# Optimization experiments

Hardware: AMD Instinct MI355X
Metric: run time of the kernel (lower is better)

Reference implementation:

```python
import jax, jax.numpy as jnp
import numpy as np


def _time_encoding(t, hidden_dim):
    # Sinusoidal continuous-time encoding: t [B,T] -> [B,T,H]
    half = hidden_dim // 2
    freqs = jnp.exp(-jnp.arange(half, dtype=t.dtype) * (np.log(10000.0) / half))
    ang = t[..., None] * freqs  # [B,T,half]
    return jnp.concatenate([jnp.sin(ang), jnp.cos(ang)], axis=-1)


def _gru(x_tbh, w_ih, w_hh, b_ih, b_hh):
    # PyTorch-convention GRU over time-major input [T,B,H]
    B = x_tbh.shape[1]
    H = w_hh.shape[1]
    h0 = jnp.zeros((B, H), x_tbh.dtype)

    def step(h, x):
        gi = x @ w_ih.T + b_ih
        gh = h @ w_hh.T + b_hh
        i_r, i_z, i_n = jnp.split(gi, 3, axis=-1)
        h_r, h_z, h_n = jnp.split(gh, 3, axis=-1)
        r = jax.nn.sigmoid(i_r + h_r)
        z = jax.nn.sigmoid(i_z + h_z)
        n = jnp.tanh(i_n + r * h_n)
        h_new = (1.0 - z) * n + z * h
        return h_new, h_new

    _, ys = jax.lax.scan(step, h0, x_tbh)
    return ys  # [T,B,H]


def setup_inputs():
    key = jax.random.key(0)
    ks = jax.random.split(key, 8)
    B, T, D, H = 32, 256, 64, 128
    x = jax.random.normal(ks[0], (B, T, D), jnp.float32)
    missing_mask = (jax.random.uniform(ks[1], (B, T, D)) < 0.5).astype(jnp.float32)
    visit_time = jnp.cumsum(jax.random.uniform(ks[2], (B, T), jnp.float32) * 2.0, axis=1)
    time_delta = jnp.zeros((B, T), jnp.float32)
    lengths = jax.random.randint(ks[3], (B,), T // 2, T + 1).astype(jnp.int32)
    lengths = lengths.at[0].set(T)  # pad_packed returns max(lengths) steps; pin to T
    sensor_embed = jax.random.normal(ks[4], (D, H), jnp.float32) * 0.02
    k = 1.0 / np.sqrt(H)
    gru_w_ih = jax.random.uniform(ks[5], (3 * H, H), jnp.float32, -k, k)
    gru_w_hh = jax.random.uniform(ks[6], (3 * H, H), jnp.float32, -k, k)
    gru_b_ih = jax.random.uniform(ks[7], (3 * H,), jnp.float32, -k, k)
    gru_b_hh = jnp.zeros((3 * H,), jnp.float32)
    return dict(x=x, missing_mask=missing_mask, visit_time=visit_time,
                time_delta=time_delta, lengths=lengths, sensor_embed=sensor_embed,
                gru_w_ih=gru_w_ih, gru_w_hh=gru_w_hh, gru_b_ih=gru_b_ih, gru_b_hh=gru_b_hh)


def reference(x, missing_mask, visit_time, time_delta, lengths, sensor_embed,
              gru_w_ih, gru_w_hh, gru_b_ih, gru_b_hh):
    B, T, D = x.shape
    H = sensor_embed.shape[1]
    observed = 1.0 - missing_mask                                   # [B,T,D]
    # sensor tokens: per-(t,sensor) embedding scaled by value, zeroed if missing
    sensor_tokens = x[..., None] * sensor_embed[None, None] * observed[..., None]  # [B,T,D,H]
    presence = observed.mean(axis=1)                                # [B,D]
    sim = jax.nn.relu(sensor_embed @ sensor_embed.T)                # [D,D]
    adj = presence[:, :, None] * presence[:, None, :] * sim[None]   # [B,D,D]
    adj = adj + jnp.eye(D, dtype=x.dtype)[None]
    adj = adj / jnp.maximum(adj.sum(axis=-1, keepdims=True), 1e-6)
    graph_tokens = jnp.einsum('bij,btjh->btih', adj, sensor_tokens) # [B,T,D,H]
    visit_repr = graph_tokens.mean(axis=2) + _time_encoding(visit_time, H)  # [B,T,H]
    # dropout is identity in eval mode
    ys = _gru(jnp.swapaxes(visit_repr, 0, 1), gru_w_ih, gru_w_hh, gru_b_ih, gru_b_hh)
    out = jnp.swapaxes(ys, 0, 1)                                    # [B,T,H]
    # pad_packed_sequence semantics: zeros beyond each sequence length
    mask = (jnp.arange(T)[None, :] < lengths[:, None])[..., None]
    return out * mask
```

## Files before the change

kernel.cpp:

```cpp
#include <hip/hip_runtime.h>
#include <hip/hip_bf16.h>

#define B_ 32
#define T_ 256
#define D_ 64
#define H_ 128
#define G_ 384

typedef _Float16 half8 __attribute__((ext_vector_type(8)));
typedef _Float16 half4v __attribute__((ext_vector_type(4)));
typedef float float4v __attribute__((ext_vector_type(4)));

__device__ __forceinline__ float fsigmoid2(float s){
  return __builtin_amdgcn_rcpf(1.0f + __builtin_amdgcn_exp2f(-s));
}
__device__ __forceinline__ float ftanh2(float t){
  return 1.0f - 2.0f*__builtin_amdgcn_rcpf(1.0f + __builtin_amdgcn_exp2f(t));
}
#define LOG2E  1.442695041f
#define LOG2E2 2.885390082f

#define BAR() do{ asm volatile("s_waitcnt lgkmcnt(0)" ::: "memory"); \
                  __builtin_amdgcn_s_barrier(); \
                  asm volatile("" ::: "memory"); } while(0)

__global__ void __launch_bounds__(256) adj_k(const float* mm, const float* E,
                                             float* wcol){
  int b = blockIdx.x;
  int tid = threadIdx.x;
  int d = tid & 63, q = tid >> 6;
  __shared__ float spp[4][64];
  __shared__ float sp[64];
  __shared__ float sE[64*129];
  __shared__ float ssim[64*65];
  __shared__ float srs[64];
  float p = 0.0f;
  for (int t = q*64; t < q*64+64; t++) p += 1.0f - mm[(b*T_ + t)*D_ + d];
  spp[q][d] = p;
  for (int i = tid; i < D_*H_; i += 256){ int r = i >> 7, c = i & 127; sE[r*129+c] = E[i]; }
  __syncthreads();
  if (tid < 64) sp[tid] = (spp[0][tid]+spp[1][tid]+spp[2][tid]+spp[3][tid]) * (1.0f/T_);
  __syncthreads();
  float rowE[128];
  #pragma unroll
  for (int k = 0; k < 128; k++) rowE[k] = sE[d*129+k];
  for (int i = q*16; i < q*16+16; i++){
    float s = 0.0f;
    #pragma unroll
    for (int k = 0; k < 128; k++) s += rowE[k]*sE[i*129+k];
    ssim[d*65+i] = fmaxf(s, 0.0f);
  }
  __syncthreads();
  if (tid < 64){
    float rs = 0.0f;
    for (int j = 0; j < 64; j++) rs += sp[j]*ssim[tid*65+j];
    srs[tid] = fmaxf(sp[tid]*rs + 1.0f, 1e-6f);
  }
  __syncthreads();
  if (tid < 64){
    float s = 0.0f;
    for (int i = 0; i < 64; i++) s += sp[i]*ssim[tid*65+i]/srs[i];
    wcol[b*64 + tid] = sp[tid]*s + 1.0f/srs[tid];
  }
}

#define AVP 72
#define VRP 136
#define SEP 132
__global__ void __launch_bounds__(512,1) gi_k(const float* x, const float* mm,
                                              const float* vt, const float* E,
                                              const float* wih, const float* bih,
                                              const float* bhh, const float* wcol,
                                              _Float16* gi3){
  int bid = blockIdx.x;
  int b = bid >> 3, t0 = (bid & 7)*32;
  int tid = threadIdx.x;
  int w = tid >> 6, l = tid & 63;
  int lq = l >> 4, lm = l & 15;

  __shared__ __align__(16) _Float16 av[32*AVP];
  __shared__ __align__(16) _Float16 vrA[32*VRP];
  __shared__ __align__(16) _Float16 sEl[64*SEP];
  __shared__ float sVt[32];

  {
    int i = tid*4, t = i >> 6, d4 = i & 63;
    long src = (long)(b*T_ + t0 + t)*D_ + d4;
    float4 xv = *(const float4*)&x[src];
    float4 mv = *(const float4*)&mm[src];
    float4 wv = *(const float4*)&wcol[b*D_ + d4];
    half4v h;
    h[0]=(_Float16)(xv.x*(1.0f-mv.x)*wv.x*(1.0f/64));
    h[1]=(_Float16)(xv.y*(1.0f-mv.y)*wv.y*(1.0f/64));
    h[2]=(_Float16)(xv.z*(1.0f-mv.z)*wv.z*(1.0f/64));
    h[3]=(_Float16)(xv.w*(1.0f-mv.w)*wv.w*(1.0f/64));
    *(half4v*)&av[t*AVP + d4] = h;
  }
  {
    int r = tid >> 3, c0 = (tid & 7)*16;
    #pragma unroll
    for (int g = 0; g < 4; g++){
      float4 v = *(const float4*)&E[r*H_ + c0 + g*4];
      half4v h;
      h[0]=(_Float16)v.x; h[1]=(_Float16)v.y; h[2]=(_Float16)v.z; h[3]=(_Float16)v.w;
      *(half4v*)&sEl[r*SEP + c0 + g*4] = h;
    }
  }
  if (tid < 32) sVt[tid] = vt[b*T_ + t0 + tid];
  __syncthreads();

  half8 bE[2];
  #pragma unroll
  for (int kc = 0; kc < 2; kc++){
    half8 f;
    #pragma unroll
    for (int jj = 0; jj < 8; jj++)
      f[jj] = sEl[(kc*32 + lq*8 + jj)*SEP + 16*w + lm];
    bE[kc] = f;
  }

  float4v accA[2] = {{0,0,0,0},{0,0,0,0}};
  #pragma unroll
  for (int kc = 0; kc < 2; kc++){
    #pragma unroll
    for (int mt = 0; mt < 2; mt++){
      half8 a = *(const half8*)&av[(mt*16+lm)*AVP + kc*32 + lq*8];
      accA[mt] = __builtin_amdgcn_mfma_f32_16x16x32_f16(a, bE[kc], accA[mt], 0,0,0);
    }
  }
  {
    int h = 16*w + lm;
    float fr = __expf(-(float)(h & 63) * 0.14391157f);
    #pragma unroll
    for (int mt = 0; mt < 2; mt++){
      #pragma unroll
      for (int r = 0; r < 4; r++){
        int tl = mt*16 + lq*4 + r;
        float ang = sVt[tl] * fr;
        float e = (h < 64) ? __sinf(ang) : __cosf(ang);
        vrA[tl*VRP + h] = (_Float16)(accA[mt][r] + e);
      }
    }
  }
  __syncthreads();

  half8 bW[3][4]; float biW[3];
  #pragma unroll
  for (int q = 0; q < 3; q++){
    int g = 16*(3*w + q) + lm;
    float sc = (g < 2*H_) ? LOG2E : LOG2E2;
    biW[q] = (bih[g] + (g < 2*H_ ? bhh[g] : 0.0f)) * sc;
    #pragma unroll
    for (int kc = 0; kc < 4; kc++){
      const float* src = &wih[(long)g*H_ + kc*32 + lq*8];
      float4 x0 = *(const float4*)src;
      float4 x1 = *(const float4*)(src+4);
      half8 f;
      f[0]=(_Float16)(x0.x*sc); f[1]=(_Float16)(x0.y*sc); f[2]=(_Float16)(x0.z*sc); f[3]=(_Float16)(x0.w*sc);
      f[4]=(_Float16)(x1.x*sc); f[5]=(_Float16)(x1.y*sc); f[6]=(_Float16)(x1.z*sc); f[7]=(_Float16)(x1.w*sc);
      bW[q][kc] = f;
    }
  }
  float4v cB[2][3];
  #pragma unroll
  for (int mt = 0; mt < 2; mt++)
    #pragma unroll
    for (int q = 0; q < 3; q++) cB[mt][q] = (float4v){0,0,0,0};
  #pragma unroll
  for (int kc = 0; kc < 4; kc++){
    #pragma unroll
    for (int mt = 0; mt < 2; mt++){
      half8 a = *(const half8*)&vrA[(mt*16+lm)*VRP + kc*32 + lq*8];
      #pragma unroll
      for (int q = 0; q < 3; q++)
        cB[mt][q] = __builtin_amdgcn_mfma_f32_16x16x32_f16(a, bW[q][kc], cB[mt][q], 0,0,0);
    }
  }
  #pragma unroll
  for (int mt = 0; mt < 2; mt++){
    #pragma unroll
    for (int q = 0; q < 3; q++){
      int g = 16*(3*w + q) + lm;
      int tb = t0 + mt*16 + lq*4;
      half4v hv;
      hv[0]=(_Float16)(cB[mt][q][0] + biW[q]); hv[1]=(_Float16)(cB[mt][q][1] + biW[q]);
      hv[2]=(_Float16)(cB[mt][q][2] + biW[q]); hv[3]=(_Float16)(cB[mt][q][3] + biW[q]);
      *(half4v*)&gi3[((long)(b*G_ + g))*T_ + tb] = hv;
    }
  }
}

__global__ void __launch_bounds__(256,1) gru_k(const _Float16* gi3, const float* whh,
                                               const float* bhh, const int* lengths,
                                               float* out){
  int b = blockIdx.x;
  int tid = threadIdx.x;
  int w = tid >> 6, l = tid & 63;
  int lq = l >> 4, lm = l & 15;
  int len = lengths[b];
  bool gate = (l < 32);
  int j = 32*w + l;

  __shared__ __align__(16) _Float16 hb[2][H_];

  half8 bfrag[6][4];
  #pragma unroll
  for (int i = 0; i < 6; i++){
    int row = 32*w + (i>>1)*H_ + (i&1)*16 + lm;
    float sc = ((i>>1) == 2) ? LOG2E2 : LOG2E;
    #pragma unroll
    for (int kc = 0; kc < 4; kc++){
      const float* src = &whh[(long)row*H_ + kc*32 + lq*8];
      float4 x0 = *(const float4*)src;
      float4 x1 = *(const float4*)(src+4);
      half8 f;
      f[0]=(_Float16)(x0.x*sc); f[1]=(_Float16)(x0.y*sc); f[2]=(_Float16)(x0.z*sc); f[3]=(_Float16)(x0.w*sc);
      f[4]=(_Float16)(x1.x*sc); f[5]=(_Float16)(x1.y*sc); f[6]=(_Float16)(x1.z*sc); f[7]=(_Float16)(x1.w*sc);
      bfrag[i][kc] = f;
    }
  }
  float bn_ = 0.0f;
  const _Float16* pr = nullptr; const _Float16* pz; const _Float16* pn;
  if (gate){
    bn_ = bhh[2*H_ + j] * LOG2E2;
    pr = gi3 + ((long)b*G_ + j)*T_;
    pz = pr + (long)H_*T_;
    pn = pr + (long)2*H_*T_;
  }
  if (tid < H_){ hb[0][tid] = (_Float16)0.0f; hb[1][tid] = (_Float16)0.0f; }

  float gr[2][8], gz[2][8], gn[2][8];
  if (gate){
    half8 a = *(const half8*)(pr);
    half8 bv = *(const half8*)(pz);
    half8 cv = *(const half8*)(pn);
    #pragma unroll
    for (int i = 0; i < 8; i++){ gr[0][i]=(float)a[i]; gz[0][i]=(float)bv[i]; gn[0][i]=(float)cv[i]; }
  }
  __syncthreads();

  float hval = 0.0f;
  float ho[8];
  int cb = 0;
  for (int c = 0; c < 32; c++){
    if (gate && c+1 < 32){
      int nb2 = (c+1)*8;
      half8 a = *(const half8*)(pr+nb2);
      half8 bv = *(const half8*)(pz+nb2);
      half8 cv = *(const half8*)(pn+nb2);
      int nc = cb^1;
      #pragma unroll
      for (int i = 0; i < 8; i++){ gr[nc][i]=(float)a[i]; gz[nc][i]=(float)bv[i]; gn[nc][i]=(float)cv[i]; }
    }
    #pragma unroll
    for (int i = 0; i < 8; i++){
      int rp = i & 1;
      half8 a0v = *(const half8*)&hb[rp][0*32 + lq*8];
      half8 a1v = *(const half8*)&hb[rp][1*32 + lq*8];
      half8 a2v = *(const half8*)&hb[rp][2*32 + lq*8];
      half8 a3v = *(const half8*)&hb[rp][3*32 + lq*8];
      float4v cc[6];
      #pragma unroll
      for (int q = 0; q < 6; q++) cc[q] = (float4v){0,0,0,0};
      #pragma unroll
      for (int q = 0; q < 6; q++) cc[q] = __builtin_amdgcn_mfma_f32_16x16x32_f16(a0v, bfrag[q][0], cc[q], 0,0,0);
      #pragma unroll
      for (int q = 0; q < 6; q++) cc[q] = __builtin_amdgcn_mfma_f32_16x16x32_f16(a1v, bfrag[q][1], cc[q], 0,0,0);
      #pragma unroll
      for (int q = 0; q < 6; q++) cc[q] = __builtin_amdgcn_mfma_f32_16x16x32_f16(a2v, bfrag[q][2], cc[q], 0,0,0);
      #pragma unroll
      for (int q = 0; q < 6; q++) cc[q] = __builtin_amdgcn_mfma_f32_16x16x32_f16(a3v, bfrag[q][3], cc[q], 0,0,0);
      float ghr = (l & 16) ? cc[1][0] : cc[0][0];
      float ghz = (l & 16) ? cc[3][0] : cc[2][0];
      float ghn = (l & 16) ? cc[5][0] : cc[4][0];
      if (gate){
        float r = fsigmoid2(gr[cb][i] + ghr);
        float z = fsigmoid2(gz[cb][i] + ghz);
        float n = ftanh2(gn[cb][i] + r*(ghn + bn_));
        hval = (1.0f - z)*n + z*hval;
        hb[rp^1][j] = (_Float16)hval;
        ho[i] = (c*8 + i < len) ? hval : 0.0f;
      }
      BAR();
    }
    if (gate){
      long ob = ((long)b*T_ + c*8)*H_ + j;
      #pragma unroll
      for (int i = 0; i < 8; i++) out[ob + (long)i*H_] = ho[i];
    }
    cb ^= 1;
  }
}

extern "C" void kernel_launch(void* const* d_in, const int* in_sizes, int n_in,
                              void* d_out, int out_size, void* d_ws, size_t ws_size,
                              hipStream_t stream) {
  char* base = (char*)d_ws;
  size_t off = 0;
  auto alloc = [&](size_t bytes)->void*{
    void* p = base + off; off = (off + bytes + 255) & ~(size_t)255; return p;
  };
  float*     wcol = (float*)alloc((size_t)B_*D_*4);
  _Float16*  gi3  = (_Float16*)alloc((size_t)B_*G_*T_*2);
  if (off > ws_size) return;

  const float* x   = (const float*)d_in[0];
  const float* mm  = (const float*)d_in[1];
  const float* vt  = (const float*)d_in[2];
  const int*   len = (const int*)d_in[4];
  const float* E   = (const float*)d_in[5];
  const float* wih = (const float*)d_in[6];
  const float* whh = (const float*)d_in[7];
  const float* bih = (const float*)d_in[8];
  const float* bhh = (const float*)d_in[9];

  adj_k<<<dim3(B_),dim3(256),0,stream>>>(mm, E, wcol);
  gi_k<<<dim3(256),dim3(512),0,stream>>>(x, mm, vt, E, wih, bih, bhh, wcol, gi3);
  gru_k<<<dim3(B_),dim3(256),0,stream>>>(gi3, whh, bhh, len, (float*)d_out);
}
```

Before: 238.7 us.

## Split GRU recurrence across eight waves with three MFMA chains each

The GRU kernel now runs with 512 threads (8 waves), so each wave owns 16 hidden units instead of 32. That halves the per-wave MFMA chain from 24 to 12 dependent-ish ops per timestep and interleaves the three gate accumulators. Gate inputs are kept as half8 registers and prefetched with a manual two-stage unroll rather than converted float arrays. The aim is a shorter critical path per serial step, at the cost of more waves joining every barrier.

New measurement: 227.7 us. -4.6%, faster.

```diff
diff --git a/kernel.cpp b/kernel.cpp
--- a/kernel.cpp
+++ b/kernel.cpp
@@ -190,24 +190,24 @@
   }
 }
 
-__global__ void __launch_bounds__(256,1) gru_k(const _Float16* gi3, const float* whh,
+__global__ void __launch_bounds__(512,1) gru_k(const _Float16* gi3, const float* whh,
                                                const float* bhh, const int* lengths,
                                                float* out){
   int b = blockIdx.x;
   int tid = threadIdx.x;
   int w = tid >> 6, l = tid & 63;
-  int lq = l >> 4, lm = l & 15;
+  int lq = l >> 4;
+  int j = 16*w + (l & 15);
+  bool gate = (l < 16);
   int len = lengths[b];
-  bool gate = (l < 32);
-  int j = 32*w + l;
 
   __shared__ __align__(16) _Float16 hb[2][H_];
 
-  half8 bfrag[6][4];
-  #pragma unroll
-  for (int i = 0; i < 6; i++){
-    int row = 32*w + (i>>1)*H_ + (i&1)*16 + lm;
-    float sc = ((i>>1) == 2) ? LOG2E2 : LOG2E;
+  half8 bfrag[3][4];
+  #pragma unroll
+  for (int q = 0; q < 3; q++){
+    int row = q*H_ + 16*w + (l & 15);
+    float sc = (q == 2) ? LOG2E2 : LOG2E;
     #pragma unroll
     for (int kc = 0; kc < 4; kc++){
       const float* src = &whh[(long)row*H_ + kc*32 + lq*8];
@@ -216,68 +216,49 @@
       half8 f;
       f[0]=(_Float16)(x0.x*sc); f[1]=(_Float16)(x0.y*sc); f[2]=(_Float16)(x0.z*sc); f[3]=(_Float16)(x0.w*sc);
       f[4]=(_Float16)(x1.x*sc); f[5]=(_Float16)(x1.y*sc); f[6]=(_Float16)(x1.z*sc); f[7]=(_Float16)(x1.w*sc);
-      bfrag[i][kc] = f;
-    }
-  }
-  float bn_ = 0.0f;
-  const _Float16* pr = nullptr; const _Float16* pz; const _Float16* pn;
-  if (gate){
-    bn_ = bhh[2*H_ + j] * LOG2E2;
-    pr = gi3 + ((long)b*G_ + j)*T_;
-    pz = pr + (long)H_*T_;
-    pn = pr + (long)2*H_*T_;
-  }
+      bfrag[q][kc] = f;
+    }
+  }
+  float bn_ = bhh[2*H_ + j] * LOG2E2;
+  const _Float16* pr = gi3 + ((long)b*G_ + j)*T_;
+  const _Float16* pz = pr + (long)H_*T_;
+  const _Float16* pn = pr + (long)2*H_*T_;
+
   if (tid < H_){ hb[0][tid] = (_Float16)0.0f; hb[1][tid] = (_Float16)0.0f; }
 
-  float gr[2][8], gz[2][8], gn[2][8];
-  if (gate){
-    half8 a = *(const half8*)(pr);
-    half8 bv = *(const half8*)(pz);
-    half8 cv = *(const half8*)(pn);
-    #pragma unroll
-    for (int i = 0; i < 8; i++){ gr[0][i]=(float)a[i]; gz[0][i]=(float)bv[i]; gn[0][i]=(float)cv[i]; }
-  }
+  half8 prA, pzA, pnA, prB, pzB, pnB;
+  prA = *(const half8*)pr; pzA = *(const half8*)pz; pnA = *(const half8*)pn;
   __syncthreads();
 
   float hval = 0.0f;
-  float ho[8];
-  int cb = 0;
-  for (int c = 0; c < 32; c++){
-    if (gate && c+1 < 32){
-      int nb2 = (c+1)*8;
-      half8 a = *(const half8*)(pr+nb2);
-      half8 bv = *(const half8*)(pz+nb2);
-      half8 cv = *(const half8*)(pn+nb2);
-      int nc = cb^1;
-      #pragma unroll
-      for (int i = 0; i < 8; i++){ gr[nc][i]=(float)a[i]; gz[nc][i]=(float)bv[i]; gn[nc][i]=(float)cv[i]; }
-    }
+
+  auto substeps = [&](half8 cr, half8 cz, half8 cn, int c){
+    float ho[8];
     #pragma unroll
     for (int i = 0; i < 8; i++){
-      int rp = i & 1;
-      half8 a0v = *(const half8*)&hb[rp][0*32 + lq*8];
-      half8 a1v = *(const half8*)&hb[rp][1*32 + lq*8];
-      half8 a2v = *(const half8*)&hb[rp][2*32 + lq*8];
-      half8 a3v = *(const half8*)&hb[rp][3*32 + lq*8];
-      float4v cc[6];
-      #pragma unroll
-      for (int q = 0; q < 6; q++) cc[q] = (float4v){0,0,0,0};
-      #pragma unroll
-      for (int q = 0; q < 6; q++) cc[q] = __builtin_amdgcn_mfma_f32_16x16x32_f16(a0v, bfrag[q][0], cc[q], 0,0,0);
-      #pragma unroll
-      for (int q = 0; q < 6; q++) cc[q] = __builtin_amdgcn_mfma_f32_16x16x32_f16(a1v, bfrag[q][1], cc[q], 0,0,0);
-      #pragma unroll
-      for (int q = 0; q < 6; q++) cc[q] = __builtin_amdgcn_mfma_f32_16x16x32_f16(a2v, bfrag[q][2], cc[q], 0,0,0);
-      #pragma unroll
-      for (int q = 0; q < 6; q++) cc[q] = __builtin_amdgcn_mfma_f32_16x16x32_f16(a3v, bfrag[q][3], cc[q], 0,0,0);
-      float ghr = (l & 16) ? cc[1][0] : cc[0][0];
-      float ghz = (l & 16) ? cc[3][0] : cc[2][0];
-      float ghn = (l & 16) ? cc[5][0] : cc[4][0];
+      const int rp = i & 1;
+      half8 a0v = *(const half8*)&hb[rp][ 0 + lq*8];
+      half8 a1v = *(const half8*)&hb[rp][32 + lq*8];
+      half8 a2v = *(const half8*)&hb[rp][64 + lq*8];
+      half8 a3v = *(const half8*)&hb[rp][96 + lq*8];
+      float4v c0 = {0,0,0,0}, c1 = {0,0,0,0}, c2 = {0,0,0,0};
+      c0 = __builtin_amdgcn_mfma_f32_16x16x32_f16(a0v, bfrag[0][0], c0, 0,0,0);
+      c1 = __builtin_amdgcn_mfma_f32_16x16x32_f16(a0v, bfrag[1][0], c1, 0,0,0);
+      c2 = __builtin_amdgcn_mfma_f32_16x16x32_f16(a0v, bfrag[2][0], c2, 0,0,0);
+      c0 = __builtin_amdgcn_mfma_f32_16x16x32_f16(a1v, bfrag[0][1], c0, 0,0,0);
+      c1 = __builtin_amdgcn_mfma_f32_16x16x32_f16(a1v, bfrag[1][1], c1, 0,0,0);
+      c2 = __builtin_amdgcn_mfma_f32_16x16x32_f16(a1v, bfrag[2][1], c2, 0,0,0);
+      c0 = __builtin_amdgcn_mfma_f32_16x16x32_f16(a2v, bfrag[0][2], c0, 0,0,0);
+      c1 = __builtin_amdgcn_mfma_f32_16x16x32_f16(a2v, bfrag[1][2], c1, 0,0,0);
+      c2 = __builtin_amdgcn_mfma_f32_16x16x32_f16(a2v, bfrag[2][2], c2, 0,0,0);
+      c0 = __builtin_amdgcn_mfma_f32_16x16x32_f16(a3v, bfrag[0][3], c0, 0,0,0);
+      c1 = __builtin_amdgcn_mfma_f32_16x16x32_f16(a3v, bfrag[1][3], c1, 0,0,0);
+      c2 = __builtin_amdgcn_mfma_f32_16x16x32_f16(a3v, bfrag[2][3], c2, 0,0,0);
+      float r = fsigmoid2((float)cr[i] + c0[0]);
+      float z = fsigmoid2((float)cz[i] + c1[0]);
+      float n = ftanh2((float)cn[i] + r*(c2[0] + bn_));
+      hval = (1.0f - z)*n + z*hval;
       if (gate){
-        float r = fsigmoid2(gr[cb][i] + ghr);
-        float z = fsigmoid2(gz[cb][i] + ghz);
-        float n = ftanh2(gn[cb][i] + r*(ghn + bn_));
-        hval = (1.0f - z)*n + z*hval;
         hb[rp^1][j] = (_Float16)hval;
         ho[i] = (c*8 + i < len) ? hval : 0.0f;
       }
@@ -288,7 +269,19 @@
       #pragma unroll
       for (int i = 0; i < 8; i++) out[ob + (long)i*H_] = ho[i];
     }
-    cb ^= 1;
+  };
+
+  for (int c = 0; c < 32; c += 2){
+    {
+      int nb = (c+1)*8;
+      prB = *(const half8*)(pr+nb); pzB = *(const half8*)(pz+nb); pnB = *(const half8*)(pn+nb);
+    }
+    substeps(prA, pzA, pnA, c);
+    if (c+2 < 32){
+      int nb = (c+2)*8;
+      prA = *(const half8*)(pr+nb); pzA = *(const half8*)(pz+nb); pnA = *(const half8*)(pn+nb);
+    }
+    substeps(prB, pzB, pnB, c+1);
   }
 }
 
@@ -316,5 +309,5 @@
 
   adj_k<<<dim3(B_),dim3(256),0,stream>>>(mm, E, wcol);
   gi_k<<<dim3(256),dim3(512),0,stream>>>(x, mm, vt, E, wih, bih, bhh, wcol, gi3);
-  gru_k<<<dim3(B_),dim3(256),0,stream>>>(gi3, whh, bhh, len, (float*)d_out);
-}
+  gru_k<<<dim3(B_),dim3(512),0,stream>>>(gi3, whh, bhh, len, (float*)d_out);
+}
```
